# Kernel optimization log

Measured on AMD Instinct MI355X. Metric: run time of the kernel, lower is better.

Reference implementation:

```python
import jax, jax.numpy as jnp
import numpy as np

D2, D1, T1, T2, D3, T3 = 120, 40, 10, 5, 3, 1


def _kaiming_uniform(key, shape):
    # torch kaiming_uniform_ with nonlinearity='relu': bound = sqrt(6/fan_in), fan_in = shape[1]
    bound = np.sqrt(6.0 / shape[1])
    return jax.random.uniform(key, shape, jnp.float32, -bound, bound)


def setup_inputs() -> dict:
    key = jax.random.key(0)
    ks = jax.random.split(key, 6)
    x = jax.random.normal(ks[0], (131072, D1, T1), jnp.float32)
    return {
        "x": x,
        "BL_W1": _kaiming_uniform(ks[1], (D2, D1)),
        "BL_W2": _kaiming_uniform(ks[2], (T1, T2)),
        "BL_B": jnp.zeros((D2, T2), jnp.float32),
        "T_W1": _kaiming_uniform(ks[3], (D3, D2)),
        "T_W": jnp.full((T2, T2), 1.0 / T2, jnp.float32),
        "T_W2": _kaiming_uniform(ks[4], (T2, T3)),
        "T_B": jnp.zeros((D3, T3), jnp.float32),
        "l": jnp.full((1,), 0.5, jnp.float32),
    }


def _max_norm(w):
    # torch max_norm_: if frobenius norm > 10, rescale to norm 10 (done under no_grad)
    n = jnp.linalg.norm(w)
    scale = jnp.where(n > 10.0, 10.0 / (1e-8 + n), 1.0)
    return w * jax.lax.stop_gradient(scale)


def reference(x, BL_W1, BL_W2, BL_B, T_W1, T_W, T_W2, T_B, l):
    # --- weight clamps performed at the top of m_btabl.forward ---
    W1a = _max_norm(BL_W1)
    W2a = _max_norm(BL_W2)
    W1b = _max_norm(T_W1)
    Wb = _max_norm(T_W)
    W2b = _max_norm(T_W2)
    lam = jnp.clip(l[0], 0.0, 1.0)  # l.data clamped to [0,1]

    # BL layer: relu(W1 @ x @ W2 + B); x: [B, D1, T1] -> [B, D2, T2]
    h = jax.nn.relu(jnp.einsum('ed,bdt->bet', W1a, x) @ W2a + BL_B)
    # dropout(0.1) is identity at inference

    # TABL layer (t1 here = T2 = 5)
    X = jnp.einsum('ed,bdt->bet', W1b, h)          # [B, D3, T2]
    eye = jnp.eye(T2, dtype=jnp.float32)
    Wm = Wb - Wb * eye + eye / T2                  # force diagonal to 1/t1
    A = jax.nn.softmax(X @ Wm, axis=-1)            # temporal attention
    X = lam * X + (1.0 - lam) * X * A              # convex combination
    y = X @ W2b + T_B                              # [B, D3, 1]

    y = jnp.squeeze(y)                             # [B, D3]
    return jax.nn.softmax(y, axis=1)
```

## Files before the change

kernel.cpp:

```cpp
#include <hip/hip_runtime.h>
#include <stdint.h>


typedef short bf16x8 __attribute__((ext_vector_type(8)));
typedef float f32x4v __attribute__((ext_vector_type(4)));

#define NTP 256
#define NTM 320

__device__ __forceinline__ unsigned short f2bf(float f) {
    unsigned int u = __float_as_uint(f);
    u += 0x7FFFu + ((u >> 16) & 1u);
    return (unsigned short)(u >> 16);
}

__device__ __forceinline__ float block_reduce_sum(float v, float* red, int tid) {
    #pragma unroll
    for (int off = 32; off > 0; off >>= 1) v += __shfl_xor(v, off, 64);
    if ((tid & 63) == 0) red[tid >> 6] = v;
    __syncthreads();
    float r = red[0] + red[1] + red[2] + red[3];
    __syncthreads();
    return r;
}

__global__ __launch_bounds__(NTP)
void prep_kernel(const float* __restrict__ W1, const float* __restrict__ W2,
                 const float* __restrict__ B,  const float* __restrict__ Tw1,
                 const float* __restrict__ Tw, const float* __restrict__ Tw2,
                 const float* __restrict__ TB, const float* __restrict__ l,
                 float* __restrict__ ws)
{
    __shared__ float red[4];
    const int tid = threadIdx.x;
    float ss;
    ss = 0.f; for (int i = tid; i < 4800; i += NTP) { float w = W1[i];  ss += w*w; }
    const float n1 = sqrtf(block_reduce_sum(ss, red, tid));
    ss = 0.f; for (int i = tid; i < 50;   i += NTP) { float w = W2[i];  ss += w*w; }
    const float n2 = sqrtf(block_reduce_sum(ss, red, tid));
    ss = 0.f; for (int i = tid; i < 360;  i += NTP) { float w = Tw1[i]; ss += w*w; }
    const float n3 = sqrtf(block_reduce_sum(ss, red, tid));
    ss = 0.f; for (int i = tid; i < 25;   i += NTP) { float w = Tw[i];  ss += w*w; }
    const float n4 = sqrtf(block_reduce_sum(ss, red, tid));
    ss = 0.f; for (int i = tid; i < 5;    i += NTP) { float w = Tw2[i]; ss += w*w; }
    const float n5 = sqrtf(block_reduce_sum(ss, red, tid));

    const float s1 = n1 > 10.f ? 10.f/(1e-8f+n1) : 1.f;
    const float s2 = n2 > 10.f ? 10.f/(1e-8f+n2) : 1.f;
    const float s3 = n3 > 10.f ? 10.f/(1e-8f+n3) : 1.f;
    const float s4 = n4 > 10.f ? 10.f/(1e-8f+n4) : 1.f;
    const float s5 = n5 > 10.f ? 10.f/(1e-8f+n5) : 1.f;

    unsigned short* img = (unsigned short*)ws;
    for (int i = tid; i < 129*48; i += NTP) {
        const int e = i / 48, k = i - e*48;
        float v = 0.f;
        if (e < 120) {
            if (k < 40)      v = W1[e*40 + k] * s1;
            else if (k < 45) v = B[e*5 + (k-40)];
        }
        img[i] = f2bf(v);
    }
    for (int i = tid; i < 512; i += NTP) {
        const int e = i >> 2, c = i & 3;
        ws[3096 + i] = (c < 3 && e < 120) ? Tw1[c*120 + e] * s3 : 0.f;
    }
    for (int i = tid; i < 36; i += NTP) {
        float v = 0.f;
        if (i < 25)      { int r = i/5, c = i - r*5; v = (r == c) ? 0.2f : Tw[i]*s4; }
        else if (i < 30) v = Tw2[i-25] * s5;
        else if (i < 33) v = TB[i-30];
        else if (i == 33){ float lv = l[0]; v = fminf(fmaxf(lv, 0.f), 1.f); }
        ws[3608 + i] = v;
    }
    for (int i = tid; i < 50; i += NTP) ws[3644 + i] = W2[i] * s2;
}

__global__ __launch_bounds__(NTM, 4)
void btabl_main(const float* __restrict__ x, const float* __restrict__ ws,
                float* __restrict__ out, int nsamp)
{
    __align__(16) __shared__ unsigned short sW1[129*48];
    __align__(16) __shared__ float          sWp[128*4];
    __align__(16) __shared__ float          sC[36];
    __align__(16) __shared__ unsigned short sZ[320*48 + 16];
    __align__(16) __shared__ float          sX3[320*3];

    const int tid  = threadIdx.x;
    const int wave = tid >> 6;
    const int lane = tid & 63;

    {
        const float4* src = (const float4*)ws;
        float4* d1 = (float4*)sW1;
        #pragma unroll
        for (int i = 0; i < 3; i++) {
            const int idx = tid + i*NTM;
            if (idx < 774) d1[idx] = src[idx];
        }
        if (tid < 128) ((float4*)sWp)[tid] = src[774 + tid];
        if (tid < 9)   ((float4*)sC)[tid]  = src[902 + tid];
    }

    {
        bf16x8 oh = {0,0,0,0,0,0,0,0};
        oh[tid % 5] = (short)0x3F80;
        *(bf16x8*)(sZ + tid*48 + 40) = oh;
    }
    __syncthreads();

    {
        const int p   = tid;
        const int s16 = p / 20;
        const int r20 = p - s16*20;
        const float* W2p = ws + 3644;

        #pragma unroll
        for (int r = 0; r < 4; r++) {
            int sG = blockIdx.x*64 + r*16 + s16;
            sG = sG < nsamp ? sG : (nsamp - 1);
            const float4* xv = (const float4*)(x + (size_t)sG*400 + r20*20);
            float xf[20];
            #pragma unroll
            for (int i = 0; i < 5; i++) {
                const float4 q = xv[i];
                xf[i*4+0] = q.x; xf[i*4+1] = q.y; xf[i*4+2] = q.z; xf[i*4+3] = q.w;
            }
            const int col0 = (r*16 + s16)*5;
            #pragma unroll
            for (int t = 0; t < 5; t++) {
                float z0 = 0.f, z1 = 0.f;
                #pragma unroll
                for (int k = 0; k < 10; k++) {
                    const float w = W2p[k*5 + t];
                    z0 = fmaf(xf[k],      w, z0);
                    z1 = fmaf(xf[10 + k], w, z1);
                }
                const unsigned int pk =
                    (unsigned int)f2bf(z0) | ((unsigned int)f2bf(z1) << 16);
                *(unsigned int*)(sZ + (col0 + t)*48 + 2*r20) = pk;
            }
        }
    }
    __syncthreads();

    const int quad = lane >> 4;
    const int m    = lane & 15;
    const int colBase = wave * 64;

    bf16x8 Bf[4][2];
    const bf16x8 z8 = {0,0,0,0,0,0,0,0};
    #pragma unroll
    for (int nt = 0; nt < 4; nt++) {
        const int col = colBase + nt*16 + m;
        Bf[nt][0] = *(const bf16x8*)(sZ + col*48 + quad*8);
        bf16x8 b1 = *(const bf16x8*)(sZ + col*48 + 32 + quad*8);
        Bf[nt][1] = (quad >= 2) ? z8 : b1;
    }

    float X3p[4][3];
    #pragma unroll
    for (int nt = 0; nt < 4; nt++)
        #pragma unroll
        for (int j = 0; j < 3; j++) X3p[nt][j] = 0.f;

    const f32x4v zacc = {0.f, 0.f, 0.f, 0.f};
    #pragma unroll
    for (int mt = 0; mt < 8; mt++) {
        const unsigned short* arow = sW1 + (mt*16 + m)*48;
        const bf16x8 A0 = *(const bf16x8*)(arow + quad*8);
        const bf16x8 A1 = *(const bf16x8*)(arow + 32 + quad*8);
        f32x4v wp[4];
        #pragma unroll
        for (int r = 0; r < 4; r++)
            wp[r] = *(const f32x4v*)(sWp + (mt*16 + quad*4 + r)*4);
        #pragma unroll
        for (int nt = 0; nt < 4; nt++) {
            f32x4v acc = __builtin_amdgcn_mfma_f32_16x16x32_bf16(A0, Bf[nt][0], zacc, 0, 0, 0);
            acc = __builtin_amdgcn_mfma_f32_16x16x32_bf16(A1, Bf[nt][1], acc, 0, 0, 0);
            #pragma unroll
            for (int r = 0; r < 4; r++) {
                const float h = fmaxf(acc[r], 0.f);
                X3p[nt][0] = fmaf(wp[r][0], h, X3p[nt][0]);
                X3p[nt][1] = fmaf(wp[r][1], h, X3p[nt][1]);
                X3p[nt][2] = fmaf(wp[r][2], h, X3p[nt][2]);
            }
        }
    }

    #pragma unroll
    for (int nt = 0; nt < 4; nt++) {
        #pragma unroll
        for (int j = 0; j < 3; j++) {
            float v = X3p[nt][j];
            v += __shfl_xor(v, 16, 64);
            v += __shfl_xor(v, 32, 64);
            X3p[nt][j] = v;
        }
    }
    if (quad == 0) {
        #pragma unroll
        for (int nt = 0; nt < 4; nt++) {
            const int col = colBase + nt*16 + m;
            sX3[col*3 + 0] = X3p[nt][0];
            sX3[col*3 + 1] = X3p[nt][1];
            sX3[col*3 + 2] = X3p[nt][2];
        }
    }
    __syncthreads();

    if (tid < 64) {
        const int sGlob = blockIdx.x * 64 + tid;
        float X3v[3][5];
        #pragma unroll
        for (int t = 0; t < 5; t++)
            #pragma unroll
            for (int j = 0; j < 3; j++)
                X3v[j][t] = sX3[(tid*5 + t)*3 + j];

        const float lam  = sC[33];
        const float olam = 1.f - lam;
        float y[3];
        #pragma unroll
        for (int j = 0; j < 3; j++) {
            float S[5];
            #pragma unroll
            for (int t = 0; t < 5; t++) {
                float a = 0.f;
                #pragma unroll
                for (int k = 0; k < 5; k++)
                    a = fmaf(X3v[j][k], sC[k*5 + t], a);
                S[t] = a;
            }
            float mx = S[0];
            #pragma unroll
            for (int t = 1; t < 5; t++) mx = fmaxf(mx, S[t]);
            float ex[5], se = 0.f;
            #pragma unroll
            for (int t = 0; t < 5; t++) { ex[t] = __expf(S[t] - mx); se += ex[t]; }
            const float inv = 1.f / se;
            float yj = sC[30 + j];
            #pragma unroll
            for (int t = 0; t < 5; t++) {
                const float a  = ex[t] * inv;
                const float xc = X3v[j][t] * (lam + olam * a);
                yj = fmaf(xc, sC[25 + t], yj);
            }
            y[j] = yj;
        }
        const float mx = fmaxf(y[0], fmaxf(y[1], y[2]));
        const float e0 = __expf(y[0]-mx), e1 = __expf(y[1]-mx), e2 = __expf(y[2]-mx);
        const float inv = 1.f / (e0 + e1 + e2);
        if (sGlob < nsamp) {
            float* o = out + (size_t)sGlob*3;
            o[0] = e0*inv; o[1] = e1*inv; o[2] = e2*inv;
        }
    }
}

extern "C" void kernel_launch(void* const* d_in, const int* in_sizes, int n_in,
                              void* d_out, int out_size, void* d_ws, size_t ws_size,
                              hipStream_t stream) {
    const float* x   = (const float*)d_in[0];
    const float* W1  = (const float*)d_in[1];
    const float* W2  = (const float*)d_in[2];
    const float* B   = (const float*)d_in[3];
    const float* Tw1 = (const float*)d_in[4];
    const float* Tw  = (const float*)d_in[5];
    const float* Tw2 = (const float*)d_in[6];
    const float* TB  = (const float*)d_in[7];
    const float* l   = (const float*)d_in[8];
    float* out = (float*)d_out;
    float* ws  = (float*)d_ws;

    hipLaunchKernelGGL(prep_kernel, dim3(1), dim3(NTP), 0, stream,
                       W1, W2, B, Tw1, Tw, Tw2, TB, l, ws);

    const int nsamp = in_sizes[0] / 400;
    const int grid  = (nsamp + 63) / 64;
    hipLaunchKernelGGL(btabl_main, dim3(grid), dim3(NTM), 0, stream,
                       x, ws, out, nsamp);
}
```

Measured before the change: 334.2 us.

## Split fused kernel into separate x@W2 pass and MFMA GEMM pass

Adds a first kernel that computes the x@W2 product per sample and writes it as bf16 into a workspace buffer laid out per 64-sample group. A second kernel loads that buffer into shared memory and runs the W1 MFMA, ReLU, projection and TABL softmax. This decouples the irregular x loading and small matmul from the MFMA stage, which may improve latency hiding and occupancy. In exchange it adds an extra global write and read of the intermediate and one more launch, and it only runs when the workspace is large enough.

```diff
diff --git a/kernel.cpp b/kernel.cpp
--- a/kernel.cpp
+++ b/kernel.cpp
@@ -76,6 +76,200 @@
     for (int i = tid; i < 50; i += NTP) ws[3644 + i] = W2[i] * s2;
 }
 
+__global__ __launch_bounds__(256)
+void zgemm_kernel(const float* __restrict__ x, const float* __restrict__ ws,
+                  unsigned short* __restrict__ zg, int nsamp)
+{
+    const int p = blockIdx.x * 256 + threadIdx.x;
+    int s = p / 20;
+    const int r20 = p - s * 20;
+    if (s >= nsamp) s = nsamp - 1;
+    const float* W2p = ws + 3644;
+
+    const float4* xv = (const float4*)(x + (size_t)s*400 + r20*20);
+    float xf[20];
+    #pragma unroll
+    for (int i = 0; i < 5; i++) {
+        const float4 q = xv[i];
+        xf[i*4+0] = q.x; xf[i*4+1] = q.y; xf[i*4+2] = q.z; xf[i*4+3] = q.w;
+    }
+
+    const int g  = s >> 6;
+    const int sl = s & 63;
+    unsigned short* zc = zg + (size_t)g*12800 + sl*200 + 2*r20;
+    #pragma unroll
+    for (int t = 0; t < 5; t++) {
+        float z0 = 0.f, z1 = 0.f;
+        #pragma unroll
+        for (int k = 0; k < 10; k++) {
+            const float w = W2p[k*5 + t];
+            z0 = fmaf(xf[k],      w, z0);
+            z1 = fmaf(xf[10 + k], w, z1);
+        }
+        *(unsigned int*)(zc + t*40) =
+            (unsigned int)f2bf(z0) | ((unsigned int)f2bf(z1) << 16);
+    }
+}
+
+__global__ __launch_bounds__(NTM)
+void btabl_gemm(const unsigned short* __restrict__ zg, const float* __restrict__ ws,
+                float* __restrict__ out, int nsamp)
+{
+    __align__(16) __shared__ unsigned short sW1[129*48];
+    __align__(16) __shared__ float          sWp[128*4];
+    __align__(16) __shared__ float          sC[36];
+    __align__(16) __shared__ unsigned short sZ[320*48 + 16];
+    __align__(16) __shared__ float          sX3[320*3];
+
+    const int tid  = threadIdx.x;
+    const int wave = tid >> 6;
+    const int lane = tid & 63;
+
+    {
+        const float4* src = (const float4*)ws;
+        float4* d1 = (float4*)sW1;
+        #pragma unroll
+        for (int i = 0; i < 3; i++) {
+            const int idx = tid + i*NTM;
+            if (idx < 774) d1[idx] = src[idx];
+        }
+        if (tid < 128) ((float4*)sWp)[tid] = src[774 + tid];
+        if (tid < 9)   ((float4*)sC)[tid]  = src[902 + tid];
+    }
+
+    {
+        bf16x8 oh = {0,0,0,0,0,0,0,0};
+        oh[tid % 5] = (short)0x3F80;
+        *(bf16x8*)(sZ + tid*48 + 40) = oh;
+    }
+
+    {
+        const int u  = tid % 5;
+        const int c0 = tid / 5;
+        const unsigned short* gsrc = zg + (size_t)blockIdx.x * 12800;
+        #pragma unroll
+        for (int i = 0; i < 5; i++) {
+            const int col = i*64 + c0;
+            const float4 v = *(const float4*)(gsrc + (size_t)col*40 + u*8);
+            *(float4*)(sZ + col*48 + u*8) = v;
+        }
+    }
+    __syncthreads();
+
+    const int quad = lane >> 4;
+    const int m    = lane & 15;
+    const int colBase = wave * 64;
+
+    bf16x8 Bf[4][2];
+    const bf16x8 z8 = {0,0,0,0,0,0,0,0};
+    #pragma unroll
+    for (int nt = 0; nt < 4; nt++) {
+        const int col = colBase + nt*16 + m;
+        Bf[nt][0] = *(const bf16x8*)(sZ + col*48 + quad*8);
+        bf16x8 b1 = *(const bf16x8*)(sZ + col*48 + 32 + quad*8);
+        Bf[nt][1] = (quad >= 2) ? z8 : b1;
+    }
+
+    float X3p[4][3];
+    #pragma unroll
+    for (int nt = 0; nt < 4; nt++)
+        #pragma unroll
+        for (int j = 0; j < 3; j++) X3p[nt][j] = 0.f;
+
+    const f32x4v zacc = {0.f, 0.f, 0.f, 0.f};
+    #pragma unroll
+    for (int mt = 0; mt < 8; mt++) {
+        const unsigned short* arow = sW1 + (mt*16 + m)*48;
+        const bf16x8 A0 = *(const bf16x8*)(arow + quad*8);
+        const bf16x8 A1 = *(const bf16x8*)(arow + 32 + quad*8);
+        f32x4v wp[4];
+        #pragma unroll
+        for (int r = 0; r < 4; r++)
+            wp[r] = *(const f32x4v*)(sWp + (mt*16 + quad*4 + r)*4);
+        #pragma unroll
+        for (int nt = 0; nt < 4; nt++) {
+            f32x4v acc = __builtin_amdgcn_mfma_f32_16x16x32_bf16(A0, Bf[nt][0], zacc, 0, 0, 0);
+            acc = __builtin_amdgcn_mfma_f32_16x16x32_bf16(A1, Bf[nt][1], acc, 0, 0, 0);
+            #pragma unroll
+            for (int r = 0; r < 4; r++) {
+                const float h = fmaxf(acc[r], 0.f);
+                X3p[nt][0] = fmaf(wp[r][0], h, X3p[nt][0]);
+                X3p[nt][1] = fmaf(wp[r][1], h, X3p[nt][1]);
+                X3p[nt][2] = fmaf(wp[r][2], h, X3p[nt][2]);
+            }
+        }
+    }
+
+    #pragma unroll
+    for (int nt = 0; nt < 4; nt++) {
+        #pragma unroll
+        for (int j = 0; j < 3; j++) {
+            float v = X3p[nt][j];
+            v += __shfl_xor(v, 16, 64);
+            v += __shfl_xor(v, 32, 64);
+            X3p[nt][j] = v;
+        }
+    }
+    if (quad == 0) {
+        #pragma unroll
+        for (int nt = 0; nt < 4; nt++) {
+            const int col = colBase + nt*16 + m;
+            sX3[col*3 + 0] = X3p[nt][0];
+            sX3[col*3 + 1] = X3p[nt][1];
+            sX3[col*3 + 2] = X3p[nt][2];
+        }
+    }
+    __syncthreads();
+
+    if (tid < 64) {
+        const int sGlob = blockIdx.x * 64 + tid;
+        float X3v[3][5];
+        #pragma unroll
+        for (int t = 0; t < 5; t++)
+            #pragma unroll
+            for (int j = 0; j < 3; j++)
+                X3v[j][t] = sX3[(tid*5 + t)*3 + j];
+
+        const float lam  = sC[33];
+        const float olam = 1.f - lam;
+        float y[3];
+        #pragma unroll
+        for (int j = 0; j < 3; j++) {
+            float S[5];
+            #pragma unroll
+            for (int t = 0; t < 5; t++) {
+                float a = 0.f;
+                #pragma unroll
+                for (int k = 0; k < 5; k++)
+                    a = fmaf(X3v[j][k], sC[k*5 + t], a);
+                S[t] = a;
+            }
+            float mx = S[0];
+            #pragma unroll
+            for (int t = 1; t < 5; t++) mx = fmaxf(mx, S[t]);
+            float ex[5], se = 0.f;
+            #pragma unroll
+            for (int t = 0; t < 5; t++) { ex[t] = __expf(S[t] - mx); se += ex[t]; }
+            const float inv = 1.f / se;
+            float yj = sC[30 + j];
+            #pragma unroll
+            for (int t = 0; t < 5; t++) {
+                const float a  = ex[t] * inv;
+                const float xc = X3v[j][t] * (lam + olam * a);
+                yj = fmaf(xc, sC[25 + t], yj);
+            }
+            y[j] = yj;
+        }
+        const float mx = fmaxf(y[0], fmaxf(y[1], y[2]));
+        const float e0 = __expf(y[0]-mx), e1 = __expf(y[1]-mx), e2 = __expf(y[2]-mx);
+        const float inv = 1.f / (e0 + e1 + e2);
+        if (sGlob < nsamp) {
+            float* o = out + (size_t)sGlob*3;
+            o[0] = e0*inv; o[1] = e1*inv; o[2] = e2*inv;
+        }
+    }
+}
+
 __global__ __launch_bounds__(NTM, 4)
 void btabl_main(const float* __restrict__ x, const float* __restrict__ ws,
                 float* __restrict__ out, int nsamp)
@@ -101,7 +295,6 @@
         if (tid < 128) ((float4*)sWp)[tid] = src[774 + tid];
         if (tid < 9)   ((float4*)sC)[tid]  = src[902 + tid];
     }
-
     {
         bf16x8 oh = {0,0,0,0,0,0,0,0};
         oh[tid % 5] = (short)0x3F80;
@@ -276,8 +469,20 @@
     hipLaunchKernelGGL(prep_kernel, dim3(1), dim3(NTP), 0, stream,
                        W1, W2, B, Tw1, Tw, Tw2, TB, l, ws);
 
-    const int nsamp = in_sizes[0] / 400;
-    const int grid  = (nsamp + 63) / 64;
-    hipLaunchKernelGGL(btabl_main, dim3(grid), dim3(NTM), 0, stream,
-                       x, ws, out, nsamp);
-}
+    const int nsamp  = in_sizes[0] / 400;
+    const int ngrp   = (nsamp + 63) / 64;
+    const size_t zoff   = 16384;
+    const size_t zbytes = (size_t)ngrp * 12800 * 2;
+
+    if (ws_size >= zoff + zbytes) {
+        unsigned short* zg = (unsigned short*)((char*)ws + zoff);
+        const int zblocks = (nsamp * 20 + 255) / 256;
+        hipLaunchKernelGGL(zgemm_kernel, dim3(zblocks), dim3(256), 0, stream,
+                           x, ws, zg, nsamp);
+        hipLaunchKernelGGL(btabl_gemm, dim3(ngrp), dim3(NTM), 0, stream,
+                           zg, ws, out, nsamp);
+    } else {
+        hipLaunchKernelGGL(btabl_main, dim3(ngrp), dim3(NTM), 0, stream,
+                           x, ws, out, nsamp);
+    }
+}
```

After: 370.4 us. 1.11x slower.

## Make each wave own 16 samples end-to-end, removing block barriers

Applied to the files above, without the earlier changes.

The block shrinks from 320 to 256 threads and each wave now handles its own 16 samples through the W2 projection, the MFMA BL layer and the TABL epilogue. Because every wave writes and reads only its own slice of shared memory, the block-wide barriers after the projection and before the epilogue are dropped. The epilogue runs on 48 lanes per wave instead of 64 threads per block, with the final softmax done through shuffles. The one-hot bias column is built in registers rather than stored to shared memory, and the row stride shrinks from 48 to 40, which lowers shared memory use. The risk is more bank conflicts from the 40-element stride, plus the per-thread x loads now use a different access pattern.

```diff
diff --git a/kernel.cpp b/kernel.cpp
--- a/kernel.cpp
+++ b/kernel.cpp
@@ -6,7 +6,7 @@
 typedef float f32x4v __attribute__((ext_vector_type(4)));
 
 #define NTP 256
-#define NTM 320
+#define NTM 256
 
 __device__ __forceinline__ unsigned short f2bf(float f) {
     unsigned int u = __float_as_uint(f);
@@ -83,8 +83,7 @@
     __align__(16) __shared__ unsigned short sW1[129*48];
     __align__(16) __shared__ float          sWp[128*4];
     __align__(16) __shared__ float          sC[36];
-    __align__(16) __shared__ unsigned short sZ[320*48 + 16];
-    __align__(16) __shared__ float          sX3[320*3];
+    __align__(16) __shared__ unsigned short sZ[320*40 + 32];
 
     const int tid  = threadIdx.x;
     const int wave = tid >> 6;
@@ -94,30 +93,23 @@
         const float4* src = (const float4*)ws;
         float4* d1 = (float4*)sW1;
         #pragma unroll
-        for (int i = 0; i < 3; i++) {
+        for (int i = 0; i < 4; i++) {
             const int idx = tid + i*NTM;
             if (idx < 774) d1[idx] = src[idx];
         }
         if (tid < 128) ((float4*)sWp)[tid] = src[774 + tid];
         if (tid < 9)   ((float4*)sC)[tid]  = src[902 + tid];
     }
+    __syncthreads();
 
     {
-        bf16x8 oh = {0,0,0,0,0,0,0,0};
-        oh[tid % 5] = (short)0x3F80;
-        *(bf16x8*)(sZ + tid*48 + 40) = oh;
-    }
-    __syncthreads();
-
-    {
-        const int p   = tid;
-        const int s16 = p / 20;
-        const int r20 = p - s16*20;
         const float* W2p = ws + 3644;
-
-        #pragma unroll
-        for (int r = 0; r < 4; r++) {
-            int sG = blockIdx.x*64 + r*16 + s16;
+        #pragma unroll
+        for (int r = 0; r < 5; r++) {
+            const int job = r*64 + lane;
+            const int sl  = job / 20;
+            const int r20 = job - sl*20;
+            int sG = blockIdx.x*64 + wave*16 + sl;
             sG = sG < nsamp ? sG : (nsamp - 1);
             const float4* xv = (const float4*)(x + (size_t)sG*400 + r20*20);
             float xf[20];
@@ -126,7 +118,7 @@
                 const float4 q = xv[i];
                 xf[i*4+0] = q.x; xf[i*4+1] = q.y; xf[i*4+2] = q.z; xf[i*4+3] = q.w;
             }
-            const int col0 = (r*16 + s16)*5;
+            const int col0 = (wave*16 + sl)*5;
             #pragma unroll
             for (int t = 0; t < 5; t++) {
                 float z0 = 0.f, z1 = 0.f;
@@ -136,31 +128,36 @@
                     z0 = fmaf(xf[k],      w, z0);
                     z1 = fmaf(xf[10 + k], w, z1);
                 }
-                const unsigned int pk =
+                *(unsigned int*)(sZ + (col0 + t)*40 + 2*r20) =
                     (unsigned int)f2bf(z0) | ((unsigned int)f2bf(z1) << 16);
-                *(unsigned int*)(sZ + (col0 + t)*48 + 2*r20) = pk;
             }
         }
     }
-    __syncthreads();
 
     const int quad = lane >> 4;
     const int m    = lane & 15;
-    const int colBase = wave * 64;
-
-    bf16x8 Bf[4][2];
+    const int colBase = wave * 80;
+
+    bf16x8 Bf0[5], Bf1[5];
     const bf16x8 z8 = {0,0,0,0,0,0,0,0};
     #pragma unroll
-    for (int nt = 0; nt < 4; nt++) {
+    for (int nt = 0; nt < 5; nt++) {
         const int col = colBase + nt*16 + m;
-        Bf[nt][0] = *(const bf16x8*)(sZ + col*48 + quad*8);
-        bf16x8 b1 = *(const bf16x8*)(sZ + col*48 + 32 + quad*8);
-        Bf[nt][1] = (quad >= 2) ? z8 : b1;
-    }
-
-    float X3p[4][3];
-    #pragma unroll
-    for (int nt = 0; nt < 4; nt++)
+        Bf0[nt] = *(const bf16x8*)(sZ + col*40 + quad*8);
+        const bf16x8 braw = *(const bf16x8*)(sZ + col*40 + (quad == 0 ? 32 : 0));
+        bf16x8 v = z8;
+        if (quad == 0) v = braw;
+        if (quad == 1) {
+            const int oh = (nt + m) % 5;
+            #pragma unroll
+            for (int j = 0; j < 5; j++) v[j] = (oh == j) ? (short)0x3F80 : (short)0;
+        }
+        Bf1[nt] = v;
+    }
+
+    float X3p[5][3];
+    #pragma unroll
+    for (int nt = 0; nt < 5; nt++)
         #pragma unroll
         for (int j = 0; j < 3; j++) X3p[nt][j] = 0.f;
 
@@ -175,9 +172,9 @@
         for (int r = 0; r < 4; r++)
             wp[r] = *(const f32x4v*)(sWp + (mt*16 + quad*4 + r)*4);
         #pragma unroll
-        for (int nt = 0; nt < 4; nt++) {
-            f32x4v acc = __builtin_amdgcn_mfma_f32_16x16x32_bf16(A0, Bf[nt][0], zacc, 0, 0, 0);
-            acc = __builtin_amdgcn_mfma_f32_16x16x32_bf16(A1, Bf[nt][1], acc, 0, 0, 0);
+        for (int nt = 0; nt < 5; nt++) {
+            f32x4v acc = __builtin_amdgcn_mfma_f32_16x16x32_bf16(A0, Bf0[nt], zacc, 0, 0, 0);
+            acc = __builtin_amdgcn_mfma_f32_16x16x32_bf16(A1, Bf1[nt], acc, 0, 0, 0);
             #pragma unroll
             for (int r = 0; r < 4; r++) {
                 const float h = fmaxf(acc[r], 0.f);
@@ -189,7 +186,7 @@
     }
 
     #pragma unroll
-    for (int nt = 0; nt < 4; nt++) {
+    for (int nt = 0; nt < 5; nt++) {
         #pragma unroll
         for (int j = 0; j < 3; j++) {
             float v = X3p[nt][j];
@@ -198,63 +195,57 @@
             X3p[nt][j] = v;
         }
     }
+    float* sX3w = (float*)(sZ + wave*3200);
     if (quad == 0) {
         #pragma unroll
-        for (int nt = 0; nt < 4; nt++) {
-            const int col = colBase + nt*16 + m;
-            sX3[col*3 + 0] = X3p[nt][0];
-            sX3[col*3 + 1] = X3p[nt][1];
-            sX3[col*3 + 2] = X3p[nt][2];
-        }
-    }
-    __syncthreads();
-
-    if (tid < 64) {
-        const int sGlob = blockIdx.x * 64 + tid;
-        float X3v[3][5];
-        #pragma unroll
-        for (int t = 0; t < 5; t++)
-            #pragma unroll
-            for (int j = 0; j < 3; j++)
-                X3v[j][t] = sX3[(tid*5 + t)*3 + j];
+        for (int nt = 0; nt < 5; nt++) {
+            const int cLoc = nt*16 + m;
+            sX3w[cLoc*3 + 0] = X3p[nt][0];
+            sX3w[cLoc*3 + 1] = X3p[nt][1];
+            sX3w[cLoc*3 + 2] = X3p[nt][2];
+        }
+    }
+
+    {
+        const int sdiv = lane / 3;
+        const int j    = lane - sdiv*3;
+        const int sLoc = sdiv & 15;
+        float X3v[5];
+        #pragma unroll
+        for (int t = 0; t < 5; t++) X3v[t] = sX3w[(sLoc*5 + t)*3 + j];
 
         const float lam  = sC[33];
         const float olam = 1.f - lam;
-        float y[3];
-        #pragma unroll
-        for (int j = 0; j < 3; j++) {
-            float S[5];
-            #pragma unroll
-            for (int t = 0; t < 5; t++) {
-                float a = 0.f;
-                #pragma unroll
-                for (int k = 0; k < 5; k++)
-                    a = fmaf(X3v[j][k], sC[k*5 + t], a);
-                S[t] = a;
-            }
-            float mx = S[0];
-            #pragma unroll
-            for (int t = 1; t < 5; t++) mx = fmaxf(mx, S[t]);
-            float ex[5], se = 0.f;
-            #pragma unroll
-            for (int t = 0; t < 5; t++) { ex[t] = __expf(S[t] - mx); se += ex[t]; }
-            const float inv = 1.f / se;
-            float yj = sC[30 + j];
-            #pragma unroll
-            for (int t = 0; t < 5; t++) {
-                const float a  = ex[t] * inv;
-                const float xc = X3v[j][t] * (lam + olam * a);
-                yj = fmaf(xc, sC[25 + t], yj);
-            }
-            y[j] = yj;
-        }
-        const float mx = fmaxf(y[0], fmaxf(y[1], y[2]));
-        const float e0 = __expf(y[0]-mx), e1 = __expf(y[1]-mx), e2 = __expf(y[2]-mx);
-        const float inv = 1.f / (e0 + e1 + e2);
-        if (sGlob < nsamp) {
-            float* o = out + (size_t)sGlob*3;
-            o[0] = e0*inv; o[1] = e1*inv; o[2] = e2*inv;
-        }
+        float S[5];
+        #pragma unroll
+        for (int t = 0; t < 5; t++) {
+            float a = 0.f;
+            #pragma unroll
+            for (int k = 0; k < 5; k++) a = fmaf(X3v[k], sC[k*5 + t], a);
+            S[t] = a;
+        }
+        float mx = S[0];
+        #pragma unroll
+        for (int t = 1; t < 5; t++) mx = fmaxf(mx, S[t]);
+        float ex[5], se = 0.f;
+        #pragma unroll
+        for (int t = 0; t < 5; t++) { ex[t] = __expf(S[t] - mx); se += ex[t]; }
+        const float inv = 1.f / se;
+        float yj = sC[30 + j];
+        #pragma unroll
+        for (int t = 0; t < 5; t++) {
+            const float a  = ex[t] * inv;
+            const float xc = X3v[t] * (lam + olam * a);
+            yj = fmaf(xc, sC[25 + t], yj);
+        }
+        const float ya = __shfl(yj, sLoc*3 + 0, 64);
+        const float yb = __shfl(yj, sLoc*3 + 1, 64);
+        const float yc = __shfl(yj, sLoc*3 + 2, 64);
+        const float my = fmaxf(ya, fmaxf(yb, yc));
+        const float sse = __expf(ya - my) + __expf(yb - my) + __expf(yc - my);
+        const float p = __expf(yj - my) / sse;
+        const int sG = blockIdx.x*64 + wave*16 + sLoc;
+        if (lane < 48 && sG < nsamp) out[(size_t)sG*3 + j] = p;
     }
 }
 
```

New measurement: 345.9 us. 3.5% more time.
